# Kernel tuning notes

Hardware: AMD Instinct MI355X
Metric: run time of the kernel (lower is better)

The kernel has to match this reference:

```python
import jax, jax.numpy as jnp
import numpy as np

B, S, DM, NH, DK, DFF = 4, 2048, 512, 8, 64, 2048
EPS = 1e-5


def setup_inputs() -> dict:
    key = jax.random.key(0)
    ks = jax.random.split(key, 16)
    sd = 1.0 / np.sqrt(DM)
    inp = {
        'x': jax.random.normal(ks[0], (B, S, DM), dtype=jnp.float32),
        'wq': jax.random.normal(ks[1], (DM, DM), dtype=jnp.float32) * sd,
        'bq': jnp.zeros((DM,), dtype=jnp.float32),
        'wk': jax.random.normal(ks[2], (DM, DM), dtype=jnp.float32) * sd,
        'bk': jnp.zeros((DM,), dtype=jnp.float32),
        'wv': jax.random.normal(ks[3], (DM, DM), dtype=jnp.float32) * sd,
        'bv': jnp.zeros((DM,), dtype=jnp.float32),
        'wo': jax.random.normal(ks[4], (DM, DM), dtype=jnp.float32) * sd,
        'bo': jnp.zeros((DM,), dtype=jnp.float32),
        'ln_g': jnp.ones((DM,), dtype=jnp.float32),
        'ln_b': jnp.zeros((DM,), dtype=jnp.float32),
        'w1': jax.random.normal(ks[5], (DFF, DM), dtype=jnp.float32) * sd,
        'b1': jnp.zeros((DFF,), dtype=jnp.float32),
        'w2': jax.random.normal(ks[6], (DM, DFF), dtype=jnp.float32) * (1.0 / np.sqrt(DFF)),
        'b2': jnp.zeros((DM,), dtype=jnp.float32),
    }
    return inp


def _layernorm(x, g, b):
    mu = jnp.mean(x, axis=-1, keepdims=True)
    var = jnp.mean(jnp.square(x - mu), axis=-1, keepdims=True)
    return (x - mu) * jax.lax.rsqrt(var + EPS) * g + b


def reference(x, wq, bq, wk, bk, wv, bv, wo, bo, ln_g, ln_b, w1, b1, w2, b2):
    # projections (torch Linear: y = x @ W.T + b)
    q = x @ wq.T + bq
    k = x @ wk.T + bk
    v = x @ wv.T + bv
    # chunk along feature dim into NH heads of size DK
    q = q.reshape(B, S, NH, DK)
    k = k.reshape(B, S, NH, DK)
    v = v.reshape(B, S, NH, DK)
    scores = jnp.einsum('bihd,bjhd->bhij', q, k) / np.sqrt(DK)  # [B,NH,S,S]
    probs = jax.nn.softmax(scores, axis=-1)
    o = jnp.einsum('bhij,bjhd->bihd', probs, v).reshape(B, S, DM)
    o = o @ wo.T + bo
    # residual + shared layernorm (dropout p=0 -> identity)
    h = _layernorm(o + x, ln_g, ln_b)
    ff = jax.nn.relu(h @ w1.T + b1) @ w2.T + b2
    return _layernorm(ff + h, ln_g, ln_b)
```

## Files before the change

kernel.cpp:

```cpp
#include <hip/hip_runtime.h>

typedef __attribute__((ext_vector_type(8))) short short8;
typedef __attribute__((ext_vector_type(8))) unsigned short ushort8;
typedef __attribute__((ext_vector_type(4))) unsigned short ushort4v;
typedef __attribute__((ext_vector_type(4))) float f32x4;

#define DEV static __device__ __forceinline__

DEV unsigned short f2bf(float f) {
  unsigned u = __builtin_bit_cast(unsigned, f);
  u += 0x7fffu + ((u >> 16) & 1u);
  return (unsigned short)(u >> 16);
}

DEV float bf2f(unsigned short u) {
  return __builtin_bit_cast(float, (unsigned)u << 16);
}

DEV void gload_lds16(const void* g, void* l) {
  __builtin_amdgcn_global_load_lds((__attribute__((address_space(1))) void*)g,
                                   (__attribute__((address_space(3))) void*)l,
                                   16, 0, 0);
}

__global__ __launch_bounds__(256) void cvt_all_k(
    const float4* __restrict__ wq, const float4* __restrict__ wk,
    const float4* __restrict__ wv, const float4* __restrict__ wo,
    const float4* __restrict__ w1, const float4* __restrict__ w2,
    const float4* __restrict__ x, ushort4v* __restrict__ wqkv,
    ushort4v* __restrict__ wob, ushort4v* __restrict__ w1b,
    ushort4v* __restrict__ w2b, ushort4v* __restrict__ xb) {
  const int i = threadIdx.x;
  const int b = blockIdx.x;
  const float4* s;
  ushort4v* d;
  size_t u;
  if (b < 256)       { s = wq; d = wqkv;          u = (size_t)b * 256 + i; }
  else if (b < 512)  { s = wk; d = wqkv + 65536;  u = (size_t)(b - 256) * 256 + i; }
  else if (b < 768)  { s = wv; d = wqkv + 131072; u = (size_t)(b - 512) * 256 + i; }
  else if (b < 1024) { s = wo; d = wob;           u = (size_t)(b - 768) * 256 + i; }
  else if (b < 2048) { s = w1; d = w1b;           u = (size_t)(b - 1024) * 256 + i; }
  else if (b < 3072) { s = w2; d = w2b;           u = (size_t)(b - 2048) * 256 + i; }
  else               { s = x;  d = xb;            u = (size_t)(b - 3072) * 256 + i; }
  float4 v = s[u];
  ushort4v o = { f2bf(v.x), f2bf(v.y), f2bf(v.z), f2bf(v.w) };
  d[u] = o;
}

__global__ void pack_bias_k(const float* __restrict__ bq, const float* __restrict__ bk,
                            const float* __restrict__ bv, float* __restrict__ o) {
  int i = threadIdx.x;
  o[i] = bq[i];
  o[512 + i] = bk[i];
  o[1024 + i] = bv[i];
}

template <int EPI>
__global__ __launch_bounds__(256) void gemm_bt(
    const unsigned short* __restrict__ A, const unsigned short* __restrict__ Bw,
    const float* __restrict__ bias, int M, int N, int K,
    unsigned short* __restrict__ outb, float* __restrict__ outf,
    const unsigned short* __restrict__ residb) {
  __shared__ __align__(16) unsigned short As[128 * 64];
  __shared__ __align__(16) unsigned short Bs[128 * 64];
  const int tid = threadIdx.x;
  const int lane = tid & 63;
  const int wv = tid >> 6;
  const int wr = wv >> 1, wc = wv & 1;
  const int lrow = lane & 15, lgrp = lane >> 4;
  const int bm = blockIdx.x * 128;
  const int bn = blockIdx.y * 128;

  f32x4 acc[4][4];
#pragma unroll
  for (int m = 0; m < 4; m++)
#pragma unroll
    for (int n = 0; n < 4; n++) acc[m][n] = (f32x4){0.f, 0.f, 0.f, 0.f};

  for (int k0 = 0; k0 < K; k0 += 64) {
    __syncthreads();
#pragma unroll
    for (int i = 0; i < 4; i++) {
      const int sb = wv * 64 + i * 256;
      const int slot = sb + lane;
      const int row = slot >> 3;
      const int cc = (slot & 7) ^ (row & 7);
      gload_lds16(A + (size_t)(bm + row) * K + k0 + cc * 8, &As[sb * 8]);
      gload_lds16(Bw + (size_t)(bn + row) * K + k0 + cc * 8, &Bs[sb * 8]);
    }
    __syncthreads();

#pragma unroll
    for (int kk = 0; kk < 2; kk++) {
      short8 af[4], bfr[4];
#pragma unroll
      for (int m = 0; m < 4; m++) {
        const int row = wr * 64 + m * 16 + lrow;
        af[m] = *(const short8*)&As[row * 64 + (((lgrp + 4 * kk) ^ (row & 7)) * 8)];
      }
#pragma unroll
      for (int n = 0; n < 4; n++) {
        const int row = wc * 64 + n * 16 + lrow;
        bfr[n] = *(const short8*)&Bs[row * 64 + (((lgrp + 4 * kk) ^ (row & 7)) * 8)];
      }
#pragma unroll
      for (int m = 0; m < 4; m++)
#pragma unroll
        for (int n = 0; n < 4; n++)
          acc[m][n] = __builtin_amdgcn_mfma_f32_16x16x32_bf16(af[m], bfr[n], acc[m][n], 0, 0, 0);
    }
  }

  if constexpr (EPI == 0) {
    const int proj = bn >> 9;
    if (proj == 2) {
      __shared__ __align__(16) unsigned short VT[128 * 136];
#pragma unroll
      for (int n = 0; n < 4; n++) {
        const int cl = wc * 64 + n * 16 + lrow;
        const float bval = bias[bn + cl];
#pragma unroll
        for (int m = 0; m < 4; m++)
#pragma unroll
          for (int r = 0; r < 4; r++)
            VT[cl * 136 + wr * 64 + m * 16 + lgrp * 4 + r] = f2bf(acc[m][n][r] + bval);
      }
      __syncthreads();
      const int j = (bn - 1024) >> 7;
      const int b = bm >> 11;
      const int sbase = bm & 2047;
      unsigned short* vout = outb + (size_t)2 * 4194304;
#pragma unroll
      for (int q = 0; q < 8; q++) {
        const int chunk = q * 256 + tid;
        const int cl = chunk >> 4, s8 = chunk & 15;
        const int head = 2 * j + (cl >> 6), d = cl & 63;
        ushort8 val = *(const ushort8*)&VT[cl * 136 + s8 * 8];
        *(ushort8*)(vout + ((size_t)(b * 8 + head) * 64 + d) * 2048 + sbase + s8 * 8) = val;
      }
    } else {
      const float qs = (proj == 0) ? 0.18033688011f : 1.0f;
#pragma unroll
      for (int m = 0; m < 4; m++) {
#pragma unroll
        for (int n = 0; n < 4; n++) {
          const int gcol = bn + wc * 64 + n * 16 + lrow;
          const float bval = bias[gcol];
          const int feat = gcol & 511;
          const int head = feat >> 6, d = feat & 63;
#pragma unroll
          for (int r = 0; r < 4; r++) {
            const int grow = bm + wr * 64 + m * 16 + lgrp * 4 + r;
            const int b = grow >> 11, s = grow & 2047;
            const int bh = b * 8 + head;
            outb[(size_t)proj * 4194304 + ((size_t)bh * 2048 + s) * 64 + d] =
                f2bf((acc[m][n][r] + bval) * qs);
          }
        }
      }
    }
  } else {
#pragma unroll
    for (int m = 0; m < 4; m++) {
#pragma unroll
      for (int n = 0; n < 4; n++) {
        const int gcol = bn + wc * 64 + n * 16 + lrow;
        const float bval = bias[gcol];
#pragma unroll
        for (int r = 0; r < 4; r++) {
          const int grow = bm + wr * 64 + m * 16 + lgrp * 4 + r;
          float v = acc[m][n][r] + bval;
          const size_t o = (size_t)grow * N + gcol;
          if constexpr (EPI == 1) {
            outb[o] = f2bf(v + bf2f(residb[o]));
          } else if constexpr (EPI == 2) {
            outb[o] = f2bf(v > 0.f ? v : 0.f);
          } else {
            outf[o] = v + bf2f(residb[o]);
          }
        }
      }
    }
  }
}

template <int EPI>
__global__ __launch_bounds__(256) void gemm_n64(
    const unsigned short* __restrict__ A, const unsigned short* __restrict__ Bw,
    const float* __restrict__ bias, int M, int N, int K,
    unsigned short* __restrict__ outb, float* __restrict__ outf,
    const unsigned short* __restrict__ residb) {
  __shared__ __align__(16) unsigned short As[128 * 64];
  __shared__ __align__(16) unsigned short Bs[64 * 64];
  const int tid = threadIdx.x;
  const int lane = tid & 63;
  const int wv = tid >> 6;
  const int lrow = lane & 15, lgrp = lane >> 4;
  const int bm = blockIdx.x * 128;
  const int bn = blockIdx.y * 64;

  f32x4 acc[2][4];
#pragma unroll
  for (int m = 0; m < 2; m++)
#pragma unroll
    for (int n = 0; n < 4; n++) acc[m][n] = (f32x4){0.f, 0.f, 0.f, 0.f};

  for (int k0 = 0; k0 < K; k0 += 64) {
    __syncthreads();
#pragma unroll
    for (int i = 0; i < 4; i++) {
      const int sb = wv * 64 + i * 256;
      const int slot = sb + lane;
      const int row = slot >> 3;
      const int cc = (slot & 7) ^ (row & 7);
      gload_lds16(A + (size_t)(bm + row) * K + k0 + cc * 8, &As[sb * 8]);
    }
#pragma unroll
    for (int i = 0; i < 2; i++) {
      const int sb = wv * 64 + i * 256;
      const int slot = sb + lane;
      const int row = slot >> 3;
      const int cc = (slot & 7) ^ (row & 7);
      gload_lds16(Bw + (size_t)(bn + row) * K + k0 + cc * 8, &Bs[sb * 8]);
    }
    __syncthreads();

#pragma unroll
    for (int kk = 0; kk < 2; kk++) {
      short8 af[2], bfr[4];
#pragma unroll
      for (int m = 0; m < 2; m++) {
        const int row = wv * 32 + m * 16 + lrow;
        af[m] = *(const short8*)&As[row * 64 + (((lgrp + 4 * kk) ^ (row & 7)) * 8)];
      }
#pragma unroll
      for (int n = 0; n < 4; n++) {
        const int row = n * 16 + lrow;
        bfr[n] = *(const short8*)&Bs[row * 64 + (((lgrp + 4 * kk) ^ (row & 7)) * 8)];
      }
#pragma unroll
      for (int m = 0; m < 2; m++)
#pragma unroll
        for (int n = 0; n < 4; n++)
          acc[m][n] = __builtin_amdgcn_mfma_f32_16x16x32_bf16(af[m], bfr[n], acc[m][n], 0, 0, 0);
    }
  }

#pragma unroll
  for (int m = 0; m < 2; m++) {
#pragma unroll
    for (int n = 0; n < 4; n++) {
      const int gcol = bn + n * 16 + lrow;
      const float bval = bias[gcol];
#pragma unroll
      for (int r = 0; r < 4; r++) {
        const int grow = bm + wv * 32 + m * 16 + lgrp * 4 + r;
        float v = acc[m][n][r] + bval;
        const size_t o = (size_t)grow * N + gcol;
        if constexpr (EPI == 1) {
          outb[o] = f2bf(v + bf2f(residb[o]));
        } else {
          outf[o] = v + bf2f(residb[o]);
        }
      }
    }
  }
}

__global__ __launch_bounds__(256) void attn_k(
    const unsigned short* __restrict__ Qg, const unsigned short* __restrict__ Kg,
    const unsigned short* __restrict__ Vg, unsigned short* __restrict__ Og) {
  __shared__ __align__(16) unsigned short Kl[64 * 64];
  __shared__ __align__(16) unsigned short Vl[64 * 64];
  __shared__ __align__(16) unsigned short Pl[4][16 * 88];
  const int tid = threadIdx.x, lane = tid & 63, wq = tid >> 6;
  const int lrow = lane & 15, lgrp = lane >> 4;
  const int bid = blockIdx.x;
  const int lin = (bid & 7) * 64 + (bid >> 3);
  const int bh = lin >> 4;
  const int q0 = (lin & 15) * 128;
  const size_t hbase = (size_t)bh * (2048 * 64);

  short8 qf[2][2];
#pragma unroll
  for (int t = 0; t < 2; t++) {
    const unsigned short* qp =
        Qg + hbase + (size_t)(q0 + t * 64 + wq * 16 + lrow) * 64 + lgrp * 8;
    qf[t][0] = *(const short8*)qp;
    qf[t][1] = *(const short8*)(qp + 32);
  }

  f32x4 oacc0[4], oacc1[4];
#pragma unroll
  for (int f = 0; f < 4; f++) {
    oacc0[f] = (f32x4){0.f, 0.f, 0.f, 0.f};
    oacc1[f] = (f32x4){0.f, 0.f, 0.f, 0.f};
  }
  float lr0[4] = {0.f, 0.f, 0.f, 0.f};
  float lr1[4] = {0.f, 0.f, 0.f, 0.f};

  for (int kt = 0; kt < 2048; kt += 64) {
    __syncthreads();
#pragma unroll
    for (int i = 0; i < 2; i++) {
      const int sb = wq * 64 + i * 256;
      const int slot = sb + lane;
      const int r = slot >> 3;
      const int c = (slot & 7) ^ (r & 7);
      gload_lds16(Kg + hbase + (size_t)(kt + r) * 64 + c * 8, &Kl[sb * 8]);
      gload_lds16(Vg + hbase + (size_t)r * 2048 + kt + c * 8, &Vl[sb * 8]);
    }
    __syncthreads();

#pragma unroll
    for (int t = 0; t < 2; t++) {
      f32x4* oacc = t ? oacc1 : oacc0;
      float* lr = t ? lr1 : lr0;
      f32x4 sc[4];
#pragma unroll
      for (int f = 0; f < 4; f++) sc[f] = (f32x4){0.f, 0.f, 0.f, 0.f};
      __builtin_amdgcn_s_setprio(1);
#pragma unroll
      for (int f = 0; f < 4; f++) {
        const int r = f * 16 + lrow;
        short8 k0f = *(const short8*)&Kl[(r * 8 + (lgrp ^ (r & 7))) * 8];
        short8 k1f = *(const short8*)&Kl[(r * 8 + ((4 | lgrp) ^ (r & 7))) * 8];
        sc[f] = __builtin_amdgcn_mfma_f32_16x16x32_bf16(qf[t][0], k0f, sc[f], 0, 0, 0);
        sc[f] = __builtin_amdgcn_mfma_f32_16x16x32_bf16(qf[t][1], k1f, sc[f], 0, 0, 0);
      }
      __builtin_amdgcn_s_setprio(0);

#pragma unroll
      for (int fp = 0; fp < 4; fp += 2) {
#pragma unroll
        for (int r = 0; r < 4; r++) {
          const float p0 = __builtin_amdgcn_exp2f(sc[fp][r]);
          const float p1 = __builtin_amdgcn_exp2f(sc[fp + 1][r]);
          lr[r] += p0 + p1;
          unsigned u;
          asm("v_cvt_pk_bf16_f32 %0, %1, %2" : "=v"(u) : "v"(p0), "v"(p1));
          Pl[wq][(lgrp * 4 + r) * 88 + lrow + 16 * fp] = (unsigned short)(u & 0xffffu);
          Pl[wq][(lgrp * 4 + r) * 88 + lrow + 16 * (fp + 1)] = (unsigned short)(u >> 16);
        }
      }

      short8 pa0 = *(const short8*)&Pl[wq][lrow * 88 + lgrp * 8];
      short8 pa1 = *(const short8*)&Pl[wq][lrow * 88 + 32 + lgrp * 8];
      __builtin_amdgcn_s_setprio(1);
#pragma unroll
      for (int f = 0; f < 4; f++) {
        const int r = f * 16 + lrow;
        short8 vb0 = *(const short8*)&Vl[(r * 8 + (lgrp ^ (r & 7))) * 8];
        short8 vb1 = *(const short8*)&Vl[(r * 8 + ((4 | lgrp) ^ (r & 7))) * 8];
        oacc[f] = __builtin_amdgcn_mfma_f32_16x16x32_bf16(pa0, vb0, oacc[f], 0, 0, 0);
        oacc[f] = __builtin_amdgcn_mfma_f32_16x16x32_bf16(pa1, vb1, oacc[f], 0, 0, 0);
      }
      __builtin_amdgcn_s_setprio(0);
    }
  }

  const int b = bh >> 3, h = bh & 7;
#pragma unroll
  for (int t = 0; t < 2; t++) {
    f32x4* oacc = t ? oacc1 : oacc0;
    float* lr = t ? lr1 : lr0;
    float inv[4];
#pragma unroll
    for (int r = 0; r < 4; r++) {
      float s = lr[r];
#pragma unroll
      for (int off = 8; off >= 1; off >>= 1) s += __shfl_xor(s, off);
      inv[r] = 1.0f / s;
    }
#pragma unroll
    for (int f = 0; f < 4; f++) {
#pragma unroll
      for (int r = 0; r < 4; r++) {
        const int row = q0 + t * 64 + wq * 16 + lgrp * 4 + r;
        Og[((size_t)(b * 2048 + row)) * 512 + h * 64 + f * 16 + lrow] =
            f2bf(oacc[f][r] * inv[r]);
      }
    }
  }
}

__global__ __launch_bounds__(64) void ln_k(const float* __restrict__ in,
                                           const float* __restrict__ g,
                                           const float* __restrict__ bb,
                                           float* __restrict__ outf) {
  const int row = blockIdx.x, lane = threadIdx.x;
  const float4* p = (const float4*)(in + (size_t)row * 512);
  float4 a = p[lane], b4 = p[lane + 64];
  float s = a.x + a.y + a.z + a.w + b4.x + b4.y + b4.z + b4.w;
#pragma unroll
  for (int off = 32; off >= 1; off >>= 1) s += __shfl_xor(s, off);
  const float mu = s * (1.f / 512.f);
  float q = 0.f;
  {
    float d;
    d = a.x - mu; q += d * d; d = a.y - mu; q += d * d;
    d = a.z - mu; q += d * d; d = a.w - mu; q += d * d;
    d = b4.x - mu; q += d * d; d = b4.y - mu; q += d * d;
    d = b4.z - mu; q += d * d; d = b4.w - mu; q += d * d;
  }
#pragma unroll
  for (int off = 32; off >= 1; off >>= 1) q += __shfl_xor(q, off);
  const float rstd = rsqrtf(q * (1.f / 512.f) + 1e-5f);
  const float4* gp = (const float4*)g;
  const float4* bp = (const float4*)bb;
  float4 g0 = gp[lane], g1 = gp[lane + 64], c0 = bp[lane], c1 = bp[lane + 64];
  float4 o0, o1;
  o0.x = (a.x - mu) * rstd * g0.x + c0.x;
  o0.y = (a.y - mu) * rstd * g0.y + c0.y;
  o0.z = (a.z - mu) * rstd * g0.z + c0.z;
  o0.w = (a.w - mu) * rstd * g0.w + c0.w;
  o1.x = (b4.x - mu) * rstd * g1.x + c1.x;
  o1.y = (b4.y - mu) * rstd * g1.y + c1.y;
  o1.z = (b4.z - mu) * rstd * g1.z + c1.z;
  o1.w = (b4.w - mu) * rstd * g1.w + c1.w;
  float4* of = (float4*)(outf + (size_t)row * 512);
  of[lane] = o0;
  of[lane + 64] = o1;
}

__global__ __launch_bounds__(64) void ln_bf_k(const unsigned short* __restrict__ in,
                                              const float* __restrict__ g,
                                              const float* __restrict__ bb,
                                              unsigned short* __restrict__ out) {
  const int row = blockIdx.x, lane = threadIdx.x;
  ushort8 v = *(const ushort8*)(in + (size_t)row * 512 + lane * 8);
  float f[8];
#pragma unroll
  for (int j = 0; j < 8; j++) f[j] = bf2f(v[j]);
  float s = 0.f;
#pragma unroll
  for (int j = 0; j < 8; j++) s += f[j];
#pragma unroll
  for (int off = 32; off >= 1; off >>= 1) s += __shfl_xor(s, off);
  const float mu = s * (1.f / 512.f);
  float q = 0.f;
#pragma unroll
  for (int j = 0; j < 8; j++) { const float d = f[j] - mu; q += d * d; }
#pragma unroll
  for (int off = 32; off >= 1; off >>= 1) q += __shfl_xor(q, off);
  const float rstd = rsqrtf(q * (1.f / 512.f) + 1e-5f);
  const float4* gp = (const float4*)g;
  const float4* bp = (const float4*)bb;
  float4 g0 = gp[lane * 2], g1 = gp[lane * 2 + 1];
  float4 c0 = bp[lane * 2], c1 = bp[lane * 2 + 1];
  const float gg[8] = {g0.x, g0.y, g0.z, g0.w, g1.x, g1.y, g1.z, g1.w};
  const float cc[8] = {c0.x, c0.y, c0.z, c0.w, c1.x, c1.y, c1.z, c1.w};
  ushort8 ov;
#pragma unroll
  for (int j = 0; j < 8; j++) ov[j] = f2bf((f[j] - mu) * rstd * gg[j] + cc[j]);
  *(ushort8*)(out + (size_t)row * 512 + lane * 8) = ov;
}

extern "C" void kernel_launch(void* const* d_in, const int* in_sizes, int n_in,
                              void* d_out, int out_size, void* d_ws, size_t ws_size,
                              hipStream_t stream) {
  const float* x = (const float*)d_in[0];
  const float* wq = (const float*)d_in[1];
  const float* bq = (const float*)d_in[2];
  const float* wk = (const float*)d_in[3];
  const float* bk = (const float*)d_in[4];
  const float* wv = (const float*)d_in[5];
  const float* bv = (const float*)d_in[6];
  const float* wo = (const float*)d_in[7];
  const float* bo = (const float*)d_in[8];
  const float* ln_g = (const float*)d_in[9];
  const float* ln_b = (const float*)d_in[10];
  const float* w1 = (const float*)d_in[11];
  const float* b1 = (const float*)d_in[12];
  const float* w2 = (const float*)d_in[13];
  const float* b2 = (const float*)d_in[14];

  unsigned short* ws_u = (unsigned short*)d_ws;
  unsigned short* wqkv = ws_u;
  unsigned short* wob = wqkv + 786432;
  unsigned short* w1b = wob + 262144;
  unsigned short* w2b = w1b + 1048576;
  unsigned short* xb = w2b + 1048576;
  unsigned short* qb = xb + 4194304;
  unsigned short* kb = qb + 4194304;
  unsigned short* vtb = kb + 4194304;
  unsigned short* ob = vtb + 4194304;
  unsigned short* s1b = ob + 4194304;
  unsigned short* hb = s1b + 4194304;
  unsigned short* f1b = qb;
  float* bqkv = (float*)(hb + 4194304);

  cvt_all_k<<<7168, 256, 0, stream>>>(
      (const float4*)wq, (const float4*)wk, (const float4*)wv, (const float4*)wo,
      (const float4*)w1, (const float4*)w2, (const float4*)x,
      (ushort4v*)wqkv, (ushort4v*)wob, (ushort4v*)w1b, (ushort4v*)w2b,
      (ushort4v*)xb);
  pack_bias_k<<<1, 512, 0, stream>>>(bq, bk, bv, bqkv);

  gemm_bt<0><<<dim3(64, 12), 256, 0, stream>>>(xb, wqkv, bqkv, 8192, 1536, 512,
                                               qb, nullptr, nullptr);
  attn_k<<<512, 256, 0, stream>>>(qb, kb, vtb, ob);
  gemm_n64<1><<<dim3(64, 8), 256, 0, stream>>>(ob, wob, bo, 8192, 512, 512,
                                               s1b, nullptr, xb);
  ln_bf_k<<<8192, 64, 0, stream>>>(s1b, ln_g, ln_b, hb);
  gemm_bt<2><<<dim3(64, 16), 256, 0, stream>>>(hb, w1b, b1, 8192, 2048, 512,
                                               f1b, nullptr, nullptr);
  gemm_n64<3><<<dim3(64, 8), 256, 0, stream>>>(f1b, w2b, b2, 8192, 512, 2048,
                                               nullptr, (float*)d_out, hb);
  ln_k<<<8192, 64, 0, stream>>>((float*)d_out, ln_g, ln_b, (float*)d_out);
}
```

Before: 178.0 us.

## Rewrite attention inner loop with 32x32 MFMA and register-resident P

Switches the attention kernel from 16x16x32 MFMAs to 32x32x16 MFMAs, computing S transposed (K·Q) so each wave owns 32 query rows. The probability tile is converted to bf16 and rearranged with cross-half-wave shuffles straight into A-operand registers, so the per-wave LDS P buffer and its store/load round trip go away. The row-sum normalization is simplified to one shuffle. This is meant to cut LDS traffic and instruction overhead, at the cost of more accumulator registers and a less coalesced output store pattern.

```diff
diff --git a/kernel.cpp b/kernel.cpp
--- a/kernel.cpp
+++ b/kernel.cpp
@@ -4,6 +4,7 @@
 typedef __attribute__((ext_vector_type(8))) unsigned short ushort8;
 typedef __attribute__((ext_vector_type(4))) unsigned short ushort4v;
 typedef __attribute__((ext_vector_type(4))) float f32x4;
+typedef __attribute__((ext_vector_type(16))) float f32x16;
 
 #define DEV static __device__ __forceinline__
 
@@ -21,6 +22,17 @@
   __builtin_amdgcn_global_load_lds((__attribute__((address_space(1))) void*)g,
                                    (__attribute__((address_space(3))) void*)l,
                                    16, 0, 0);
+}
+
+DEV unsigned cvtpk(float lo, float hi) {
+  unsigned u;
+  asm("v_cvt_pk_bf16_f32 %0, %1, %2" : "=v"(u) : "v"(lo), "v"(hi));
+  return u;
+}
+
+DEV short8 pack4(unsigned a, unsigned b, unsigned c, unsigned d) {
+  int4 t = make_int4((int)a, (int)b, (int)c, (int)d);
+  return __builtin_bit_cast(short8, t);
 }
 
 __global__ __launch_bounds__(256) void cvt_all_k(
@@ -272,32 +284,27 @@
     const unsigned short* __restrict__ Vg, unsigned short* __restrict__ Og) {
   __shared__ __align__(16) unsigned short Kl[64 * 64];
   __shared__ __align__(16) unsigned short Vl[64 * 64];
-  __shared__ __align__(16) unsigned short Pl[4][16 * 88];
   const int tid = threadIdx.x, lane = tid & 63, wq = tid >> 6;
-  const int lrow = lane & 15, lgrp = lane >> 4;
+  const int ql = lane & 31;
+  const int hi = lane >> 5;
   const int bid = blockIdx.x;
   const int lin = (bid & 7) * 64 + (bid >> 3);
   const int bh = lin >> 4;
   const int q0 = (lin & 15) * 128;
+  const int qw = q0 + wq * 32;
   const size_t hbase = (size_t)bh * (2048 * 64);
 
-  short8 qf[2][2];
-#pragma unroll
-  for (int t = 0; t < 2; t++) {
-    const unsigned short* qp =
-        Qg + hbase + (size_t)(q0 + t * 64 + wq * 16 + lrow) * 64 + lgrp * 8;
-    qf[t][0] = *(const short8*)qp;
-    qf[t][1] = *(const short8*)(qp + 32);
-  }
-
-  f32x4 oacc0[4], oacc1[4];
-#pragma unroll
-  for (int f = 0; f < 4; f++) {
-    oacc0[f] = (f32x4){0.f, 0.f, 0.f, 0.f};
-    oacc1[f] = (f32x4){0.f, 0.f, 0.f, 0.f};
-  }
-  float lr0[4] = {0.f, 0.f, 0.f, 0.f};
-  float lr1[4] = {0.f, 0.f, 0.f, 0.f};
+  short8 qreg[4];
+  {
+    const unsigned short* qp = Qg + hbase + (size_t)(qw + ql) * 64 + hi * 8;
+#pragma unroll
+    for (int i = 0; i < 4; i++) qreg[i] = *(const short8*)(qp + 16 * i);
+  }
+
+  f32x16 oac0 = {0.f, 0.f, 0.f, 0.f, 0.f, 0.f, 0.f, 0.f,
+                 0.f, 0.f, 0.f, 0.f, 0.f, 0.f, 0.f, 0.f};
+  f32x16 oac1 = oac0;
+  float lr = 0.f;
 
   for (int kt = 0; kt < 2048; kt += 64) {
     __syncthreads();
@@ -312,75 +319,71 @@
     }
     __syncthreads();
 
-#pragma unroll
-    for (int t = 0; t < 2; t++) {
-      f32x4* oacc = t ? oacc1 : oacc0;
-      float* lr = t ? lr1 : lr0;
-      f32x4 sc[4];
-#pragma unroll
-      for (int f = 0; f < 4; f++) sc[f] = (f32x4){0.f, 0.f, 0.f, 0.f};
-      __builtin_amdgcn_s_setprio(1);
-#pragma unroll
-      for (int f = 0; f < 4; f++) {
-        const int r = f * 16 + lrow;
-        short8 k0f = *(const short8*)&Kl[(r * 8 + (lgrp ^ (r & 7))) * 8];
-        short8 k1f = *(const short8*)&Kl[(r * 8 + ((4 | lgrp) ^ (r & 7))) * 8];
-        sc[f] = __builtin_amdgcn_mfma_f32_16x16x32_bf16(qf[t][0], k0f, sc[f], 0, 0, 0);
-        sc[f] = __builtin_amdgcn_mfma_f32_16x16x32_bf16(qf[t][1], k1f, sc[f], 0, 0, 0);
-      }
-      __builtin_amdgcn_s_setprio(0);
-
-#pragma unroll
-      for (int fp = 0; fp < 4; fp += 2) {
-#pragma unroll
-        for (int r = 0; r < 4; r++) {
-          const float p0 = __builtin_amdgcn_exp2f(sc[fp][r]);
-          const float p1 = __builtin_amdgcn_exp2f(sc[fp + 1][r]);
-          lr[r] += p0 + p1;
-          unsigned u;
-          asm("v_cvt_pk_bf16_f32 %0, %1, %2" : "=v"(u) : "v"(p0), "v"(p1));
-          Pl[wq][(lgrp * 4 + r) * 88 + lrow + 16 * fp] = (unsigned short)(u & 0xffffu);
-          Pl[wq][(lgrp * 4 + r) * 88 + lrow + 16 * (fp + 1)] = (unsigned short)(u >> 16);
-        }
-      }
-
-      short8 pa0 = *(const short8*)&Pl[wq][lrow * 88 + lgrp * 8];
-      short8 pa1 = *(const short8*)&Pl[wq][lrow * 88 + 32 + lgrp * 8];
-      __builtin_amdgcn_s_setprio(1);
-#pragma unroll
-      for (int f = 0; f < 4; f++) {
-        const int r = f * 16 + lrow;
-        short8 vb0 = *(const short8*)&Vl[(r * 8 + (lgrp ^ (r & 7))) * 8];
-        short8 vb1 = *(const short8*)&Vl[(r * 8 + ((4 | lgrp) ^ (r & 7))) * 8];
-        oacc[f] = __builtin_amdgcn_mfma_f32_16x16x32_bf16(pa0, vb0, oacc[f], 0, 0, 0);
-        oacc[f] = __builtin_amdgcn_mfma_f32_16x16x32_bf16(pa1, vb1, oacc[f], 0, 0, 0);
-      }
-      __builtin_amdgcn_s_setprio(0);
-    }
-  }
+    f32x16 sc0 = {0.f, 0.f, 0.f, 0.f, 0.f, 0.f, 0.f, 0.f,
+                  0.f, 0.f, 0.f, 0.f, 0.f, 0.f, 0.f, 0.f};
+    f32x16 sc1 = sc0;
+    __builtin_amdgcn_s_setprio(1);
+#pragma unroll
+    for (int i = 0; i < 4; i++) {
+      const int c8 = 2 * i + hi;
+      const int r0 = ql;
+      const int r1 = ql + 32;
+      short8 ka = *(const short8*)&Kl[(r0 * 8 + (c8 ^ (r0 & 7))) * 8];
+      short8 kb = *(const short8*)&Kl[(r1 * 8 + (c8 ^ (r1 & 7))) * 8];
+      sc0 = __builtin_amdgcn_mfma_f32_32x32x16_bf16(ka, qreg[i], sc0, 0, 0, 0);
+      sc1 = __builtin_amdgcn_mfma_f32_32x32x16_bf16(kb, qreg[i], sc1, 0, 0, 0);
+    }
+    __builtin_amdgcn_s_setprio(0);
+
+    short8 pa[4];
+#pragma unroll
+    for (int t2 = 0; t2 < 2; t2++) {
+      const f32x16& sc = t2 ? sc1 : sc0;
+      float p[16];
+#pragma unroll
+      for (int r = 0; r < 16; r++) {
+        p[r] = __builtin_amdgcn_exp2f(sc[r]);
+        lr += p[r];
+      }
+      unsigned w0a = cvtpk(p[0], p[1]),  w0b = cvtpk(p[2], p[3]);
+      unsigned w1a = cvtpk(p[4], p[5]),  w1b = cvtpk(p[6], p[7]);
+      unsigned w2a = cvtpk(p[8], p[9]),  w2b = cvtpk(p[10], p[11]);
+      unsigned w3a = cvtpk(p[12], p[13]), w3b = cvtpk(p[14], p[15]);
+      unsigned ea = hi ? w0a : w1a, eb = hi ? w0b : w1b;
+      unsigned ra = (unsigned)__shfl_xor((int)ea, 32);
+      unsigned rb = (unsigned)__shfl_xor((int)eb, 32);
+      pa[2 * t2] = hi ? pack4(ra, rb, w1a, w1b) : pack4(w0a, w0b, ra, rb);
+      ea = hi ? w2a : w3a; eb = hi ? w2b : w3b;
+      ra = (unsigned)__shfl_xor((int)ea, 32);
+      rb = (unsigned)__shfl_xor((int)eb, 32);
+      pa[2 * t2 + 1] = hi ? pack4(ra, rb, w3a, w3b) : pack4(w2a, w2b, ra, rb);
+    }
+
+    __builtin_amdgcn_s_setprio(1);
+#pragma unroll
+    for (int ks = 0; ks < 4; ks++) {
+      const int c8 = 2 * ks + hi;
+      const int r0 = ql;
+      const int r1 = ql + 32;
+      short8 vb0 = *(const short8*)&Vl[(r0 * 8 + (c8 ^ (r0 & 7))) * 8];
+      short8 vb1 = *(const short8*)&Vl[(r1 * 8 + (c8 ^ (r1 & 7))) * 8];
+      oac0 = __builtin_amdgcn_mfma_f32_32x32x16_bf16(pa[ks], vb0, oac0, 0, 0, 0);
+      oac1 = __builtin_amdgcn_mfma_f32_32x32x16_bf16(pa[ks], vb1, oac1, 0, 0, 0);
+    }
+    __builtin_amdgcn_s_setprio(0);
+  }
+
+  lr += __shfl_xor(lr, 32);
+  const float inv = 1.0f / lr;
 
   const int b = bh >> 3, h = bh & 7;
 #pragma unroll
-  for (int t = 0; t < 2; t++) {
-    f32x4* oacc = t ? oacc1 : oacc0;
-    float* lr = t ? lr1 : lr0;
-    float inv[4];
-#pragma unroll
-    for (int r = 0; r < 4; r++) {
-      float s = lr[r];
-#pragma unroll
-      for (int off = 8; off >= 1; off >>= 1) s += __shfl_xor(s, off);
-      inv[r] = 1.0f / s;
-    }
-#pragma unroll
-    for (int f = 0; f < 4; f++) {
-#pragma unroll
-      for (int r = 0; r < 4; r++) {
-        const int row = q0 + t * 64 + wq * 16 + lgrp * 4 + r;
-        Og[((size_t)(b * 2048 + row)) * 512 + h * 64 + f * 16 + lrow] =
-            f2bf(oacc[f][r] * inv[r]);
-      }
-    }
+  for (int r = 0; r < 16; r++) {
+    const int qrow = (r & 3) + 8 * (r >> 2) + 4 * hi;
+    const float invr = __shfl(inv, qrow);
+    const size_t base = ((size_t)(b * 2048 + qw + qrow)) * 512 + h * 64 + ql;
+    Og[base] = f2bf(oac0[r] * invr);
+    Og[base + 32] = f2bf(oac1[r] * invr);
   }
 }
 
```

New measurement: 171.7 us. -3.6%, faster.
